# Kernel optimization log

Measured on AMD Instinct MI355X. Metric: run time of the kernel, lower is better.

The kernel has to match this reference:

```python
import jax, jax.numpy as jnp
import numpy as np

B, V, C, D = 32, 64, 32, 256
VOCAB = 20000
NUM_T = 1000


def _run_lstm(x, Wih, Whh, b):
    # x: [T, B, H_in]; torch-style single-layer LSTM with zero initial state
    T, Bb, _ = x.shape
    H = Whh.shape[1]
    def step(carry, xt):
        h, c = carry
        z = xt @ Wih.T + h @ Whh.T + b
        i, f, g, o = jnp.split(z, 4, axis=-1)
        c = jax.nn.sigmoid(f) * c + jax.nn.sigmoid(i) * jnp.tanh(g)
        h = jax.nn.sigmoid(o) * jnp.tanh(c)
        return (h, c), h
    h0 = jnp.zeros((Bb, H), x.dtype)
    _, ys = jax.lax.scan(step, (h0, h0), x)
    return ys


def _forward(input_seqs, masks, lengths, seq_time_step, code_masks, emb, WQ1, WK1,
             decay, initial, lstm_Wih, lstm_Whh, lstm_b, hs_Wih, hs_Whh, hs_b,
             whk_W, whk_b, w1_W, w1_b, w2_W, w2_b, fuse_W, fuse_b, lab_W, lab_b,
             betas, Wdiff, diffusion_time_t, normal_noise):
    Bb, Vv, Cc = input_seqs.shape
    tok = input_seqs.reshape(-1, Cc)                      # [B*V, C]
    x = emb[tok]                                          # [B*V, C, D]
    q = x @ WQ1.T
    k = x @ WK1.T
    dp = jnp.einsum('bcd,bed->bce', q, k)                 # [B*V, C, C]
    cm = code_masks.reshape(-1, Cc)
    dp = dp - cm[:, None, :] - cm[:, :, None]
    sp = jax.nn.softmax(dp / jnp.sqrt(jnp.float32(D)), axis=-1)
    femb = jnp.einsum('bce,bed->bcd', sp, x)              # attended code embeddings
    femb = ((cm - 1e20) / -1e20)[:, :, None] * femb       # zero out padded codes
    dec = decay[tok][..., None]                           # [B*V, C, 1]
    ini = initial[tok][..., None]
    t = seq_time_step.reshape(-1)[:, None, None]          # [B*V, 1, 1]
    gate = jax.nn.sigmoid(dec * t + ini)                  # time-decay gate
    vv = jnp.einsum('bcx,bcd->bd', gate, femb)            # [B*V, D] visit vector
    vv = vv.reshape(Bb, Vv, -1).transpose(1, 0, 2)        # [V, B, D]

    lstm_out = _run_lstm(vv, lstm_Wih, lstm_Whh, lstm_b)  # [V, B, D]
    t_lstm = lstm_out.transpose(1, 0, 2)                  # [B, V, D]
    hiddenstate = _run_lstm(lstm_out, hs_Wih, hs_Whh, hs_b).transpose(1, 0, 2)

    # Vectorized form of the original per-step python loop.
    # NOTE: the original always uses e_k = t_lstm_out[:, 0:1, :] (step 0) -- kept faithfully.
    e_k = t_lstm[:, 0:1, :]                               # [B, 1, D]
    whp = hiddenstate[:, :-1, :] @ whk_W.T + whk_b        # [B, V-1, D]
    cat = jnp.concatenate([jnp.broadcast_to(e_k, whp.shape), whp], axis=-1)
    attn = jax.nn.softmax(jnp.tanh(cat @ w1_W.T + w1_b) @ w2_W.T + w2_b, axis=-1)
    rest = e_k * attn[..., 0:1] + whp * attn[..., 1:2]
    aligned = jnp.concatenate([e_k, rest], axis=1)        # [B, V, D]

    alpha = jnp.cumprod(1.0 - betas)[diffusion_time_t][:, None, None]
    noisy = aligned * jnp.sqrt(alpha) + normal_noise * jnp.sqrt(1.0 - alpha)
    predicted_noise = noisy @ Wdiff                       # surrogate for UNetModel (source not provided)
    gen = aligned + (normal_noise - predicted_noise)

    fused = jnp.concatenate([t_lstm, gen], axis=-1) @ fuse_W.T + fuse_b   # [B, V, D]
    mask_final = (jnp.arange(Vv)[None, :] == (lengths - 1)[:, None]).astype(fused.dtype)
    final = (fused * mask_final[:, :, None]).sum(axis=1)  # select last valid visit
    return final @ lab_W.T + lab_b                        # [B, 2]


def setup_inputs() -> dict:
    key = jax.random.key(0)
    ks = jax.random.split(key, 20)
    s = 0.05
    n = lambda i, shp: jax.random.normal(ks[i], shp, jnp.float32) * s
    emb = jax.random.normal(ks[0], (VOCAB + 1, D), jnp.float32) * 0.02
    emb = emb.at[VOCAB].set(0.0)  # padding_idx row
    return {
        'input_seqs': jax.random.randint(ks[1], (B, V, C), 0, VOCAB),
        'masks': jnp.zeros((B, V), jnp.float32),
        'lengths': jax.random.randint(ks[2], (B,), 1, V + 1),
        'seq_time_step': jax.random.uniform(ks[3], (B, V), jnp.float32),
        'code_masks': jnp.zeros((B, V, C), jnp.float32),
        'emb': emb,
        'WQ1': n(4, (D, D)), 'WK1': n(5, (D, D)),
        'decay': jnp.full((VOCAB + 1,), -0.1, jnp.float32),
        'initial': jnp.full((VOCAB + 1,), 1.0, jnp.float32),
        'lstm_Wih': n(6, (4 * D, D)), 'lstm_Whh': n(7, (4 * D, D)),
        'lstm_b': jnp.zeros((4 * D,), jnp.float32),
        'hs_Wih': n(8, (4 * D, D)), 'hs_Whh': n(9, (4 * D, D)),
        'hs_b': jnp.zeros((4 * D,), jnp.float32),
        'whk_W': n(10, (D, D)), 'whk_b': jnp.zeros((D,), jnp.float32),
        'w1_W': n(11, (64, 2 * D)), 'w1_b': jnp.zeros((64,), jnp.float32),
        'w2_W': n(12, (2, 64)), 'w2_b': jnp.zeros((2,), jnp.float32),
        'fuse_W': n(13, (D, 2 * D)), 'fuse_b': jnp.zeros((D,), jnp.float32),
        'lab_W': n(14, (2, D)), 'lab_b': jnp.zeros((2,), jnp.float32),
        'betas': jnp.linspace(1e-4, 0.02, NUM_T, dtype=jnp.float32),
        'Wdiff': n(15, (D, D)),
        'diffusion_time_t': jax.random.randint(ks[16], (B,), 0, NUM_T),
        'normal_noise': jax.random.normal(ks[17], (B, V, D), jnp.float32),
    }


def reference(input_seqs, masks, lengths, seq_time_step, code_masks, emb, WQ1, WK1,
              decay, initial, lstm_Wih, lstm_Whh, lstm_b, hs_Wih, hs_Whh, hs_b,
              whk_W, whk_b, w1_W, w1_b, w2_W, w2_b, fuse_W, fuse_b, lab_W, lab_b,
              betas, Wdiff, diffusion_time_t, normal_noise):
    return _forward(input_seqs, masks, lengths, seq_time_step, code_masks, emb, WQ1, WK1,
                    decay, initial, lstm_Wih, lstm_Whh, lstm_b, hs_Wih, hs_Whh, hs_b,
                    whk_W, whk_b, w1_W, w1_b, w2_W, w2_b, fuse_W, fuse_b, lab_W, lab_b,
                    betas, Wdiff, diffusion_time_t, normal_noise)
```

## Files before the change

### kernel.cpp

```cpp
#include <hip/hip_runtime.h>
#include <hip/hip_bf16.h>
#include <cmath>

typedef __attribute__((ext_vector_type(8))) short bf16x8;
typedef __attribute__((ext_vector_type(4))) float f32x4;
typedef __attribute__((ext_vector_type(4))) int i32x4;
typedef __attribute__((ext_vector_type(2))) unsigned int u32x2;

__device__ __forceinline__ float bf2f(unsigned short u) {
    unsigned int x = ((unsigned int)u) << 16;
    return __builtin_bit_cast(float, x);
}
__device__ __forceinline__ unsigned short f2bf(float f) {
    unsigned int x = __builtin_bit_cast(unsigned int, f);
    unsigned int lsb = (x >> 16) & 1u;
    x += 0x7fffu + lsb;
    return (unsigned short)(x >> 16);
}
__device__ __forceinline__ float sigm(float z) {
    return 1.f / (1.f + __expf(-z));
}
__device__ __forceinline__ float rcpf(float x) { return __builtin_amdgcn_rcpf(x); }
__device__ __forceinline__ float sigm_f(float z) { return rcpf(1.f + __expf(-z)); }
__device__ __forceinline__ float tanh_f(float z) { return 1.f - 2.f * rcpf(1.f + __expf(2.f * z)); }

__device__ __forceinline__ long ldg_sc8l(const void* p) {
    long r;
    asm volatile("global_load_dwordx2 %0, %1, off sc1" : "=v"(r) : "v"(p) : "memory");
    return r;
}
__device__ __forceinline__ u32x2 ldg_sc_u2(const void* p) {
    u32x2 r;
    asm volatile("global_load_dwordx2 %0, %1, off sc1" : "=v"(r) : "v"(p) : "memory");
    return r;
}
__device__ __forceinline__ void stg_sc_u2(void* p, u32x2 v) {
    asm volatile("global_store_dwordx2 %0, %1, off sc1" :: "v"(p), "v"(v) : "memory");
}
__device__ __forceinline__ void stg_sc_b(void* p, int v) {
    asm volatile("global_store_byte %0, %1, off sc1" :: "v"(p), "v"(v) : "memory");
}

__global__ void __launch_bounds__(256) pack_all(
    const float* __restrict__ Whh1, const float* __restrict__ Wih2,
    const float* __restrict__ Whh2, const float* __restrict__ Wih1,
    const float* __restrict__ WQ1, const float* __restrict__ WK1,
    const float* __restrict__ betas, const int* __restrict__ dift,
    const float* __restrict__ whk_W, const float* __restrict__ fuse_W,
    const float* __restrict__ w1_W,
    long* __restrict__ Wq, float* __restrict__ cs,
    unsigned short* __restrict__ W1h, unsigned short* __restrict__ M_pk,
    float* __restrict__ alpha, int* __restrict__ flags,
    float* __restrict__ whkT, float* __restrict__ fuseT,
    float* __restrict__ w1T) {
    int blk = blockIdx.x, tid = threadIdx.x;
    if (blk < 384) {
        int R = blk * 8 + (tid >> 5);
        int mat = R >> 10;
        int n = R & 1023;
        int t32 = tid & 31;
        const float* src = (mat == 0) ? Whh1 : (mat == 1 ? Wih2 : Whh2);
        const float* rp = src + (size_t)n * 256 + t32 * 8;
        float v[8];
        float mx = 0.f;
        for (int j = 0; j < 8; ++j) { v[j] = rp[j]; mx = fmaxf(mx, fabsf(v[j])); }
        for (int m = 1; m <= 16; m <<= 1) mx = fmaxf(mx, __shfl_xor(mx, m));
        float inv = mx > 0.f ? 127.f / mx : 0.f;
        unsigned int lo = 0, hi = 0;
        for (int j = 0; j < 4; ++j) {
            int iv = __float2int_rn(v[j] * inv);
            lo |= ((unsigned int)(unsigned char)(signed char)iv) << (8 * j);
            int iv2 = __float2int_rn(v[4 + j] * inv);
            hi |= ((unsigned int)(unsigned char)(signed char)iv2) << (8 * j);
        }
        int g = n >> 8, rem = n & 255;
        int w8 = rem >> 5, dt = (rem >> 4) & 1, cc = rem & 15;
        int t8 = g * 2 + dt;
        int kb = t32 >> 2, q = t32 & 3;
        unsigned int* dst = (unsigned int*)Wq +
            ((size_t)((mat * 512 + w8 * 64 + t8 * 8 + kb) * 64) + q * 16 + cc) * 2;
        dst[0] = lo;
        dst[1] = hi;
        if (t32 == 0) cs[mat * 1024 + n] = mx / 16129.f;
    } else if (blk < 512) {
        int cch = (blk - 384) * 256 + tid;
        int nt = cch >> 9;
        int r = cch & 511;
        int kb = r >> 6;
        int lane = r & 63;
        int grow = nt * 16 + (lane & 15);
        int k0 = kb * 32 + (lane >> 4) * 8;
        const float* sp = Wih1 + (size_t)grow * 256 + k0;
        bf16x8 hi;
        for (int j = 0; j < 8; ++j) hi[j] = (short)f2bf(sp[j]);
        *reinterpret_cast<bf16x8*>(W1h + (size_t)cch * 8) = hi;
    } else if (blk == 512) {
        if (tid < 32) {
            int tb = dift[tid];
            float p = 1.f;
            for (int i = 0; i <= tb; ++i) p *= (1.f - betas[i]);
            alpha[tid] = p;
        }
    } else if (blk == 513) {
        for (int i = tid; i < 2048; i += 256) flags[i] = 0;
    } else if (blk < 578) {
        int gid = (blk - 514) * 256 + tid;
        for (int i = 0; i < 4; ++i) {
            int e = gid + i * 16384;
            int k = e >> 8, dd = e & 255;
            whkT[e] = whk_W[(size_t)dd * 256 + k];
        }
    } else if (blk < 706) {
        int gid = (blk - 578) * 256 + tid;
        for (int i = 0; i < 4; ++i) {
            int e = gid + i * 32768;
            int k = e >> 8, dd = e & 255;
            fuseT[e] = fuse_W[(size_t)dd * 512 + k];
        }
    } else if (blk < 738) {
        int gid = (blk - 706) * 256 + tid;
        for (int i = 0; i < 4; ++i) {
            int e = gid + i * 8192;
            int k = e >> 6, j = e & 63;
            w1T[e] = w1_W[(size_t)j * 512 + k];
        }
    } else {
        __shared__ unsigned short As[256][32];
        __shared__ unsigned short Bs[256][32];
        int bx = blk - 738;
        int e0 = (bx >> 3) << 5;
        int f0 = (bx & 7) << 5;
        int col = tid & 31, rr = tid >> 5;
        for (int rep = 0; rep < 32; ++rep) {
            int d = rep * 8 + rr;
            As[d][col] = f2bf(WQ1[d * 256 + e0 + col]);
            Bs[d][col] = f2bf(WK1[d * 256 + f0 + col]);
        }
        __syncthreads();
        int el = tid & 31;
        int fl0 = tid >> 5;
        for (int i = 0; i < 4; ++i) {
            int fl = fl0 + 8 * i;
            float acc = 0.f;
            for (int d = 0; d < 256; ++d)
                acc += bf2f(As[d][el]) * bf2f(Bs[d][fl]);
            int e = e0 + el, f = f0 + fl;
            int kb = e >> 5, r = (e >> 3) & 3, j = e & 7;
            int nb = f >> 4;
            int lane = (r << 4) | (f & 15);
            M_pk[(((nb * 8 + kb) * 64) + lane) * 8 + j] = f2bf(acc);
        }
    }
}

__global__ void __launch_bounds__(256) attn_bags(
    const int* __restrict__ seqs, const float* __restrict__ tstep,
    const float* __restrict__ cmask, const float* __restrict__ emb,
    const float* __restrict__ decay, const float* __restrict__ initial,
    const unsigned short* __restrict__ M_pk, float* __restrict__ vv) {
    __shared__ __align__(16) unsigned short x_bf[32 * 256];
    __shared__ __align__(16) unsigned short t1_bf[32 * 256];
    __shared__ float dp_f[32 * 33];
    __shared__ float gate_sh[32];
    __shared__ float cm_sh[32];
    __shared__ int tok_sh[32];
    __shared__ float w_sh[32];

    int bag = blockIdx.x;
    int tid = threadIdx.x;

    if (tid < 32) {
        int tok = seqs[bag * 32 + tid];
        tok_sh[tid] = tok;
        float cm = cmask[bag * 32 + tid];
        cm_sh[tid] = cm;
        float tt = tstep[bag];
        float g = sigm(decay[tok] * tt + initial[tok]);
        g *= (cm - 1e20f) / (-1e20f);
        gate_sh[tid] = g;
    }
    __syncthreads();

    for (int it = 0; it < 8; ++it) {
        int fidx = it * 256 + tid;
        int c = fidx >> 6;
        int f4 = fidx & 63;
        const float4* src = reinterpret_cast<const float4*>(emb + (size_t)tok_sh[c] * 256) + f4;
        float4 vx = *src;
        int colx = f4 * 4;
        int eidx = c * 256 + (colx ^ ((c & 7) << 3));
        ushort4 w;
        w.x = f2bf(vx.x); w.y = f2bf(vx.y); w.z = f2bf(vx.z); w.w = f2bf(vx.w);
        *reinterpret_cast<ushort4*>(&x_bf[eidx]) = w;
    }
    __syncthreads();

    int wv = tid >> 6;
    int lane = tid & 63;
    int lr = lane & 15;
    int lk = lane >> 4;

    f32x4 acc[2][4];
    for (int a = 0; a < 2; ++a)
        for (int n = 0; n < 4; ++n) acc[a][n] = (f32x4){0.f, 0.f, 0.f, 0.f};
    for (int kb = 0; kb < 8; ++kb) {
        bf16x8 afr[2];
        for (int mb = 0; mb < 2; ++mb) {
            int row = mb * 16 + lr;
            int colx = kb * 32 + lk * 8;
            afr[mb] = *reinterpret_cast<const bf16x8*>(&x_bf[row * 256 + (colx ^ ((row & 7) << 3))]);
        }
        for (int nbi = 0; nbi < 4; ++nbi) {
            int nb = wv * 4 + nbi;
            bf16x8 bfr = *reinterpret_cast<const bf16x8*>(M_pk + (((nb * 8 + kb) * 64) + lane) * 8);
            acc[0][nbi] = __builtin_amdgcn_mfma_f32_16x16x32_bf16(afr[0], bfr, acc[0][nbi], 0, 0, 0);
            acc[1][nbi] = __builtin_amdgcn_mfma_f32_16x16x32_bf16(afr[1], bfr, acc[1][nbi], 0, 0, 0);
        }
    }
    for (int mb = 0; mb < 2; ++mb)
        for (int nbi = 0; nbi < 4; ++nbi)
            for (int r = 0; r < 4; ++r) {
                int row = mb * 16 + lk * 4 + r;
                int colx = wv * 64 + nbi * 16 + lr;
                t1_bf[row * 256 + (colx ^ ((row & 7) << 3))] = f2bf(acc[mb][nbi][r]);
            }
    __syncthreads();

    {
        int mb = wv >> 1, nb2 = wv & 1;
        f32x4 dacc = (f32x4){0.f, 0.f, 0.f, 0.f};
        for (int kb = 0; kb < 8; ++kb) {
            int cola = kb * 32 + lk * 8;
            int rowa = mb * 16 + lr;
            bf16x8 afr = *reinterpret_cast<const bf16x8*>(&t1_bf[rowa * 256 + (cola ^ ((rowa & 7) << 3))]);
            int rowb = nb2 * 16 + lr;
            bf16x8 bfr = *reinterpret_cast<const bf16x8*>(&x_bf[rowb * 256 + (cola ^ ((rowb & 7) << 3))]);
            dacc = __builtin_amdgcn_mfma_f32_16x16x32_bf16(afr, bfr, dacc, 0, 0, 0);
        }
        for (int r = 0; r < 4; ++r) {
            int c = mb * 16 + lk * 4 + r;
            int e = nb2 * 16 + lr;
            dp_f[c * 33 + e] = dacc[r];
        }
    }
    __syncthreads();

    if (tid < 32) {
        int c = tid;
        float cmc = cm_sh[c];
        float lg[32];
        float mx = -1e30f;
        for (int e = 0; e < 32; ++e) {
            float l = (dp_f[c * 33 + e] - cmc - cm_sh[e]) * 0.0625f;
            lg[e] = l;
            mx = fmaxf(mx, l);
        }
        float s = 0.f;
        for (int e = 0; e < 32; ++e) { float ex = __expf(lg[e] - mx); lg[e] = ex; s += ex; }
        float inv = 1.f / s;
        for (int e = 0; e < 32; ++e) dp_f[c * 33 + e] = lg[e] * inv;
    }
    __syncthreads();
    if (tid < 32) {
        int e = tid;
        float a2 = 0.f;
        for (int c = 0; c < 32; ++c) a2 += gate_sh[c] * dp_f[c * 33 + e];
        w_sh[e] = a2;
    }
    __syncthreads();

    float accv = 0.f;
    int d = tid;
    for (int e = 0; e < 32; ++e)
        accv += w_sh[e] * bf2f(x_bf[e * 256 + (d ^ ((e & 7) << 3))]);
    vv[(size_t)bag * 256 + d] = accv;
}

__global__ void __launch_bounds__(256) x1_mfma(const float* __restrict__ vv,
                                               const unsigned short* __restrict__ W1h,
                                               const float* __restrict__ lstm_b,
                                               unsigned short* __restrict__ X1bf) {
    __shared__ __align__(16) unsigned short xs[32 * 256];
    int blk = blockIdx.x;
    int rb = blk >> 3, gb = blk & 7;
    int tid = threadIdx.x;
    for (int it = 0; it < 8; ++it) {
        int idx = it * 256 + tid;
        int row = idx >> 6, f4 = idx & 63;
        float4 v = *reinterpret_cast<const float4*>(vv + (size_t)(rb * 32 + row) * 256 + f4 * 4);
        ushort4 w;
        w.x = f2bf(v.x); w.y = f2bf(v.y); w.z = f2bf(v.z); w.w = f2bf(v.w);
        *reinterpret_cast<ushort4*>(&xs[row * 256 + ((f4 * 4) ^ ((row & 7) << 3))]) = w;
    }
    __syncthreads();
    int wv = tid >> 6, lane = tid & 63, cl = lane & 15, kh = lane >> 4;
    f32x4 acc[2][2];
    for (int n = 0; n < 2; ++n) {
        int nt = gb * 8 + wv * 2 + n;
        float bz = lstm_b[nt * 16 + cl];
        acc[n][0] = (f32x4){bz, bz, bz, bz};
        acc[n][1] = (f32x4){bz, bz, bz, bz};
    }
    #pragma unroll
    for (int kb = 0; kb < 8; ++kb) {
        int k = kb * 32 + kh * 8;
        bf16x8 a0 = *reinterpret_cast<const bf16x8*>(&xs[cl * 256 + (k ^ ((cl & 7) << 3))]);
        bf16x8 a1 = *reinterpret_cast<const bf16x8*>(&xs[(16 + cl) * 256 + (k ^ (((16 + cl) & 7) << 3))]);
        for (int n = 0; n < 2; ++n) {
            int nt = gb * 8 + wv * 2 + n;
            size_t o = ((size_t)(nt * 8 + kb) * 64 + lane) * 8;
            bf16x8 bh = *reinterpret_cast<const bf16x8*>(W1h + o);
            acc[n][0] = __builtin_amdgcn_mfma_f32_16x16x32_bf16(a0, bh, acc[n][0], 0, 0, 0);
            acc[n][1] = __builtin_amdgcn_mfma_f32_16x16x32_bf16(a1, bh, acc[n][1], 0, 0, 0);
        }
    }
    for (int n = 0; n < 2; ++n) {
        int nt = gb * 8 + wv * 2 + n;
        int g = nt * 16 + cl;
        int dX = g & 255, gt = g >> 8;
        for (int mt = 0; mt < 2; ++mt)
            for (int r = 0; r < 4; ++r) {
                int row = rb * 32 + mt * 16 + kh * 4 + r;
                int b = row >> 6, t = row & 63;
                X1bf[((size_t)t * 32 + b) * 1024 + dX * 4 + gt] = f2bf(acc[n][mt][r]);
            }
    }
}

__global__ void __launch_bounds__(512, 2) lstm_persist(
    const long* __restrict__ Wq, const float* __restrict__ cs,
    const unsigned short* __restrict__ X1bf, const float* __restrict__ hs_b,
    unsigned short* __restrict__ h1bf, unsigned short* __restrict__ h2bf,
    signed char* h1q, unsigned short* p1, int* flags) {
    int role = blockIdx.x;
    int half = role & 1;
    int kind = role >> 1;
    int tid = threadIdx.x;
    int w = tid >> 6, lane = tid & 63, c = lane & 15, q = lane >> 4;

    long wt[64];
    #pragma unroll
    for (int t8 = 0; t8 < 8; ++t8)
        #pragma unroll
        for (int kb = 0; kb < 8; ++kb)
            wt[t8 * 8 + kb] = Wq[(size_t)((kind * 512 + w * 64 + t8 * 8 + kb) * 64) + lane];
    float csv[8];
    #pragma unroll
    for (int t8 = 0; t8 < 8; ++t8) {
        int g = t8 >> 1, dt = t8 & 1;
        csv[t8] = cs[kind * 1024 + g * 256 + w * 32 + dt * 16 + c];
    }

    if (kind == 0) {
        __shared__ signed char hq[2][16][272];
        float cstate[8] = {0.f, 0.f, 0.f, 0.f, 0.f, 0.f, 0.f, 0.f};
        int B0 = half * 16 + q * 4;
        int dbase = w * 32;
        for (int t = 0; t < 64; ++t) {
            ushort4 xv[8];
            #pragma unroll
            for (int dt = 0; dt < 2; ++dt)
                #pragma unroll
                for (int r = 0; r < 4; ++r) {
                    int B = B0 + r, d = dbase + dt * 16 + c;
                    xv[dt * 4 + r] = *reinterpret_cast<const ushort4*>(
                        X1bf + ((size_t)(t * 32 + B) * 1024 + d * 4));
                }
            i32x4 acc[8];
            #pragma unroll
            for (int i = 0; i < 8; ++i) acc[i] = (i32x4){0, 0, 0, 0};
            if (t > 0) {
                int pb = (t - 1) & 1;
                long a[8];
                #pragma unroll
                for (int kb = 0; kb < 8; ++kb)
                    a[kb] = *reinterpret_cast<const long*>(&hq[pb][c][kb * 32 + q * 8]);
                #pragma unroll
                for (int t8 = 0; t8 < 8; ++t8)
                    #pragma unroll
                    for (int kb = 0; kb < 8; ++kb)
                        acc[t8] = __builtin_amdgcn_mfma_i32_16x16x32_i8(
                            a[kb], wt[t8 * 8 + kb], acc[t8], 0, 0, 0);
            }
            #pragma unroll
            for (int dt = 0; dt < 2; ++dt)
                #pragma unroll
                for (int r = 0; r < 4; ++r) {
                    int idx = dt * 4 + r;
                    ushort4 x = xv[idx];
                    float zi = (float)acc[0 + dt][r] * csv[0 + dt] + bf2f(x.x);
                    float zf = (float)acc[2 + dt][r] * csv[2 + dt] + bf2f(x.y);
                    float zg = (float)acc[4 + dt][r] * csv[4 + dt] + bf2f(x.z);
                    float zo = (float)acc[6 + dt][r] * csv[6 + dt] + bf2f(x.w);
                    float cn = sigm_f(zf) * cstate[idx] + sigm_f(zi) * tanh_f(zg);
                    float hn = sigm_f(zo) * tanh_f(cn);
                    cstate[idx] = cn;
                    int B = B0 + r, d = dbase + dt * 16 + c;
                    h1bf[(size_t)(t * 32 + B) * 256 + d] = f2bf(hn);
                    int hv = __float2int_rn(hn * 127.f);
                    hq[t & 1][q * 4 + r][d] = (signed char)hv;
                    stg_sc_b(h1q + (size_t)(t * 32 + B) * 256 + d, hv);
                }
            asm volatile("s_waitcnt vmcnt(0)" ::: "memory");
            if (lane == 0)
                __hip_atomic_store(flags + t * 16 + half * 8 + w, 1,
                                   __ATOMIC_RELAXED, __HIP_MEMORY_SCOPE_AGENT);
            __syncthreads();
        }
    } else if (kind == 1) {
        for (int s = 0; s < 64; ++s) {
            const int* f = flags + s * 16 + half * 8;
            while (1) {
                int v = 1;
                if (lane < 8)
                    v = __hip_atomic_load(f + lane, __ATOMIC_RELAXED, __HIP_MEMORY_SCOPE_AGENT);
                if (__all(v != 0)) break;
                __builtin_amdgcn_s_sleep(1);
            }
            __builtin_amdgcn_sched_barrier(0);
            const signed char* hb = h1q + (size_t)(s * 32 + half * 16) * 256;
            long a[8];
            #pragma unroll
            for (int kb = 0; kb < 8; ++kb)
                a[kb] = ldg_sc8l(hb + c * 256 + kb * 32 + q * 8);
            asm volatile("s_waitcnt vmcnt(0)" ::: "memory");
            __builtin_amdgcn_sched_barrier(0);
            i32x4 acc[8];
            #pragma unroll
            for (int i = 0; i < 8; ++i) acc[i] = (i32x4){0, 0, 0, 0};
            #pragma unroll
            for (int t8 = 0; t8 < 8; ++t8)
                #pragma unroll
                for (int kb = 0; kb < 8; ++kb)
                    acc[t8] = __builtin_amdgcn_mfma_i32_16x16x32_i8(
                        a[kb], wt[t8 * 8 + kb], acc[t8], 0, 0, 0);
            #pragma unroll
            for (int t8 = 0; t8 < 8; ++t8) {
                int g = t8 >> 1, dt = t8 & 1;
                int n = g * 256 + w * 32 + dt * 16 + c;
                u32x2 pv;
                pv.x = (unsigned int)f2bf((float)acc[t8][0] * csv[t8]) |
                       ((unsigned int)f2bf((float)acc[t8][1] * csv[t8]) << 16);
                pv.y = (unsigned int)f2bf((float)acc[t8][2] * csv[t8]) |
                       ((unsigned int)f2bf((float)acc[t8][3] * csv[t8]) << 16);
                stg_sc_u2(p1 + ((size_t)(s * 2 + half) * 1024 + n) * 16 + q * 4, pv);
            }
            asm volatile("s_waitcnt vmcnt(0)" ::: "memory");
            if (lane == 0)
                __hip_atomic_store(flags + 1024 + s * 16 + half * 8 + w, 1,
                                   __ATOMIC_RELAXED, __HIP_MEMORY_SCOPE_AGENT);
        }
    } else {
        __shared__ signed char hq2[2][16][272];
        float cstate[8] = {0.f, 0.f, 0.f, 0.f, 0.f, 0.f, 0.f, 0.f};
        float bias[8];
        #pragma unroll
        for (int t8 = 0; t8 < 8; ++t8) {
            int g = t8 >> 1, dt = t8 & 1;
            bias[t8] = hs_b[g * 256 + w * 32 + dt * 16 + c];
        }
        int B0 = half * 16 + q * 4;
        int dbase = w * 32;
        for (int s = 0; s < 64; ++s) {
            const int* fp = flags + 1024 + s * 16 + half * 8 + w;
            while (__hip_atomic_load(fp, __ATOMIC_RELAXED, __HIP_MEMORY_SCOPE_AGENT) == 0)
                __builtin_amdgcn_s_sleep(1);
            __builtin_amdgcn_sched_barrier(0);
            u32x2 pv[8];
            #pragma unroll
            for (int t8 = 0; t8 < 8; ++t8) {
                int g = t8 >> 1, dt = t8 & 1;
                int n = g * 256 + w * 32 + dt * 16 + c;
                pv[t8] = ldg_sc_u2(p1 + ((size_t)(s * 2 + half) * 1024 + n) * 16 + q * 4);
            }
            i32x4 acc[8];
            #pragma unroll
            for (int i = 0; i < 8; ++i) acc[i] = (i32x4){0, 0, 0, 0};
            if (s > 0) {
                int pb = (s - 1) & 1;
                long a[8];
                #pragma unroll
                for (int kb = 0; kb < 8; ++kb)
                    a[kb] = *reinterpret_cast<const long*>(&hq2[pb][c][kb * 32 + q * 8]);
                asm volatile("s_waitcnt vmcnt(0)" ::: "memory");
                __builtin_amdgcn_sched_barrier(0);
                #pragma unroll
                for (int t8 = 0; t8 < 8; ++t8)
                    #pragma unroll
                    for (int kb = 0; kb < 8; ++kb)
                        acc[t8] = __builtin_amdgcn_mfma_i32_16x16x32_i8(
                            a[kb], wt[t8 * 8 + kb], acc[t8], 0, 0, 0);
            } else {
                asm volatile("s_waitcnt vmcnt(0)" ::: "memory");
                __builtin_amdgcn_sched_barrier(0);
            }
            #pragma unroll
            for (int dt = 0; dt < 2; ++dt)
                #pragma unroll
                for (int r = 0; r < 4; ++r) {
                    int idx = dt * 4 + r;
                    float p_i = bf2f((unsigned short)((r < 2 ? pv[0 + dt].x : pv[0 + dt].y) >> ((r & 1) * 16)));
                    float p_f = bf2f((unsigned short)((r < 2 ? pv[2 + dt].x : pv[2 + dt].y) >> ((r & 1) * 16)));
                    float p_g = bf2f((unsigned short)((r < 2 ? pv[4 + dt].x : pv[4 + dt].y) >> ((r & 1) * 16)));
                    float p_o = bf2f((unsigned short)((r < 2 ? pv[6 + dt].x : pv[6 + dt].y) >> ((r & 1) * 16)));
                    float zi = (float)acc[0 + dt][r] * csv[0 + dt] + p_i + bias[0 + dt];
                    float zf = (float)acc[2 + dt][r] * csv[2 + dt] + p_f + bias[2 + dt];
                    float zg = (float)acc[4 + dt][r] * csv[4 + dt] + p_g + bias[4 + dt];
                    float zo = (float)acc[6 + dt][r] * csv[6 + dt] + p_o + bias[6 + dt];
                    float cn = sigm_f(zf) * cstate[idx] + sigm_f(zi) * tanh_f(zg);
                    float hn = sigm_f(zo) * tanh_f(cn);
                    cstate[idx] = cn;
                    int B = B0 + r, d = dbase + dt * 16 + c;
                    h2bf[(size_t)(s * 32 + B) * 256 + d] = f2bf(hn);
                    hq2[s & 1][q * 4 + r][d] = (signed char)__float2int_rn(hn * 127.f);
                }
            __syncthreads();
        }
    }
}

__global__ void __launch_bounds__(256) tail_k(
    const int* __restrict__ lengths,
    const unsigned short* __restrict__ h1, const unsigned short* __restrict__ h2,
    const float* __restrict__ whkT, const float* __restrict__ whk_b,
    const float* __restrict__ w1T, const float* __restrict__ w1_b,
    const float* __restrict__ w2_W, const float* __restrict__ w2_b,
    const float* __restrict__ fuseT, const float* __restrict__ fuse_b,
    const float* __restrict__ lab_W, const float* __restrict__ lab_b,
    const float* __restrict__ Wdiff, const float* __restrict__ alpha,
    const float* __restrict__ noise, float* __restrict__ out) {
    __shared__ float ek[256], tv[256], hs[256], whp[256], a1s[64];
    __shared__ float noisy_s[256], fin[512], fused_s[256], attn_s[2];
    int b = blockIdx.x, tid = threadIdx.x;
    int vstar = lengths[b] - 1;
    {
        ek[tid] = bf2f(h1[(size_t)b * 256 + tid]);
        tv[tid] = bf2f(h1[((size_t)vstar * 32 + b) * 256 + tid]);
        if (vstar > 0)
            hs[tid] = bf2f(h2[((size_t)(vstar - 1) * 32 + b) * 256 + tid]);
    }
    __syncthreads();

    float aligned;
    if (vstar > 0) {
        float s0 = 0.f, s1 = 0.f, s2 = 0.f, s3 = 0.f;
        for (int k = 0; k < 256; k += 4) {
            s0 += whkT[(k + 0) * 256 + tid] * hs[k + 0];
            s1 += whkT[(k + 1) * 256 + tid] * hs[k + 1];
            s2 += whkT[(k + 2) * 256 + tid] * hs[k + 2];
            s3 += whkT[(k + 3) * 256 + tid] * hs[k + 3];
        }
        whp[tid] = whk_b[tid] + s0 + s1 + s2 + s3;
        __syncthreads();
        if (tid < 64) {
            float a0 = 0.f, a1 = 0.f, a2 = 0.f, a3 = 0.f;
            for (int k = 0; k < 256; k += 4) {
                a0 += w1T[(k + 0) * 64 + tid] * ek[k + 0];
                a1 += w1T[(k + 1) * 64 + tid] * ek[k + 1];
                a2 += w1T[(k + 2) * 64 + tid] * ek[k + 2];
                a3 += w1T[(k + 3) * 64 + tid] * ek[k + 3];
            }
            for (int k = 0; k < 256; k += 4) {
                a0 += w1T[(256 + k + 0) * 64 + tid] * whp[k + 0];
                a1 += w1T[(256 + k + 1) * 64 + tid] * whp[k + 1];
                a2 += w1T[(256 + k + 2) * 64 + tid] * whp[k + 2];
                a3 += w1T[(256 + k + 3) * 64 + tid] * whp[k + 3];
            }
            a1s[tid] = tanhf(w1_b[tid] + a0 + a1 + a2 + a3);
        }
        __syncthreads();
        if (tid < 2) {
            float a3 = w2_b[tid];
            const float* wr2 = w2_W + tid * 64;
            for (int k = 0; k < 64; ++k) a3 += wr2[k] * a1s[k];
            attn_s[tid] = a3;
        }
        __syncthreads();
        float m = fmaxf(attn_s[0], attn_s[1]);
        float e0 = __expf(attn_s[0] - m), e1 = __expf(attn_s[1] - m);
        float inv = 1.f / (e0 + e1);
        aligned = ek[tid] * (e0 * inv) + whp[tid] * (e1 * inv);
    } else {
        aligned = ek[tid];
    }

    float al = alpha[b];
    float sa = sqrtf(al), sb = sqrtf(1.f - al);
    float nz = noise[((size_t)b * 64 + vstar) * 256 + tid];
    noisy_s[tid] = aligned * sa + nz * sb;
    __syncthreads();
    {
        float p0 = 0.f, p1v = 0.f, p2 = 0.f, p3 = 0.f;
        for (int k = 0; k < 256; k += 4) {
            p0 += noisy_s[k + 0] * Wdiff[(size_t)(k + 0) * 256 + tid];
            p1v += noisy_s[k + 1] * Wdiff[(size_t)(k + 1) * 256 + tid];
            p2 += noisy_s[k + 2] * Wdiff[(size_t)(k + 2) * 256 + tid];
            p3 += noisy_s[k + 3] * Wdiff[(size_t)(k + 3) * 256 + tid];
        }
        float gen = aligned + nz - (p0 + p1v + p2 + p3);
        fin[tid] = tv[tid];
        fin[256 + tid] = gen;
    }
    __syncthreads();
    {
        float f0 = 0.f, f1 = 0.f, f2 = 0.f, f3 = 0.f;
        for (int k = 0; k < 512; k += 4) {
            f0 += fuseT[(k + 0) * 256 + tid] * fin[k + 0];
            f1 += fuseT[(k + 1) * 256 + tid] * fin[k + 1];
            f2 += fuseT[(k + 2) * 256 + tid] * fin[k + 2];
            f3 += fuseT[(k + 3) * 256 + tid] * fin[k + 3];
        }
        fused_s[tid] = fuse_b[tid] + f0 + f1 + f2 + f3;
    }
    __syncthreads();
    if (tid < 2) {
        float o = lab_b[tid];
        const float* lw = lab_W + tid * 256;
        for (int k = 0; k < 256; ++k) o += lw[k] * fused_s[k];
        out[b * 2 + tid] = o;
    }
}

extern "C" void kernel_launch(void* const* d_in, const int* in_sizes, int n_in,
                              void* d_out, int out_size, void* d_ws, size_t ws_size,
                              hipStream_t stream) {
    const int*   seqs    = (const int*)  d_in[0];
    const int*   lengths = (const int*)  d_in[2];
    const float* tstep   = (const float*)d_in[3];
    const float* cmask   = (const float*)d_in[4];
    const float* emb     = (const float*)d_in[5];
    const float* WQ1     = (const float*)d_in[6];
    const float* WK1     = (const float*)d_in[7];
    const float* decay   = (const float*)d_in[8];
    const float* initial = (const float*)d_in[9];
    const float* Wih1    = (const float*)d_in[10];
    const float* Whh1    = (const float*)d_in[11];
    const float* lstm_b  = (const float*)d_in[12];
    const float* Wih2    = (const float*)d_in[13];
    const float* Whh2    = (const float*)d_in[14];
    const float* hs_b    = (const float*)d_in[15];
    const float* whk_W   = (const float*)d_in[16];
    const float* whk_b   = (const float*)d_in[17];
    const float* w1_W    = (const float*)d_in[18];
    const float* w1_b    = (const float*)d_in[19];
    const float* w2_W    = (const float*)d_in[20];
    const float* w2_b    = (const float*)d_in[21];
    const float* fuse_W  = (const float*)d_in[22];
    const float* fuse_b  = (const float*)d_in[23];
    const float* lab_W   = (const float*)d_in[24];
    const float* lab_b   = (const float*)d_in[25];
    const float* betas   = (const float*)d_in[26];
    const float* Wdiff   = (const float*)d_in[27];
    const int*   dift    = (const int*)  d_in[28];
    const float* noise   = (const float*)d_in[29];
    float* out = (float*)d_out;

    float* ws = (float*)d_ws;
    size_t off = 0;
    auto alloc = [&](size_t nfloats) { size_t r = off; off += (nfloats + 63) & ~(size_t)63; return r; };
    unsigned short* M_pk  = (unsigned short*)(ws + alloc(32768));
    float*          alpha = ws + alloc(64);
    float*          cs    = ws + alloc(3072);
    int*            flags = (int*)(ws + alloc(2048));
    float*          vv    = ws + alloc(524288);
    unsigned short* X1bf  = (unsigned short*)(ws + alloc(1048576));
    unsigned short* h1bf  = (unsigned short*)(ws + alloc(262144));
    unsigned short* h2bf  = (unsigned short*)(ws + alloc(262144));
    unsigned short* p1    = (unsigned short*)(ws + alloc(1048576));
    long*           Wq    = (long*)(ws + alloc(196608));
    unsigned short* W1h   = (unsigned short*)(ws + alloc(131072));
    float*          whkT  = ws + alloc(65536);
    float*          fuseT = ws + alloc(131072);
    float*          w1T   = ws + alloc(32768);
    signed char*    h1q   = (signed char*)vv;

    pack_all<<<802, 256, 0, stream>>>(Whh1, Wih2, Whh2, Wih1, WQ1, WK1, betas, dift,
                                      whk_W, fuse_W, w1_W,
                                      Wq, cs, W1h, M_pk, alpha, flags,
                                      whkT, fuseT, w1T);
    attn_bags<<<2048, 256, 0, stream>>>(seqs, tstep, cmask, emb, decay, initial, M_pk, vv);
    x1_mfma<<<512, 256, 0, stream>>>(vv, W1h, lstm_b, X1bf);
    lstm_persist<<<6, 512, 0, stream>>>(Wq, cs, X1bf, hs_b, h1bf, h2bf, h1q, p1, flags);
    tail_k<<<32, 256, 0, stream>>>(lengths, h1bf, h2bf, whkT, whk_b,
                                   w1T, w1_b, w2_W, w2_b, fuseT, fuse_b,
                                   lab_W, lab_b, Wdiff, alpha, noise, out);
}
```

Before: 340.9 us.

## Precompute projected embedding table once instead of per-bag token projections

```diff
diff --git a/kernel.cpp b/kernel.cpp
--- a/kernel.cpp
+++ b/kernel.cpp
@@ -102,7 +102,7 @@
             alpha[tid] = p;
         }
     } else if (blk == 513) {
-        for (int i = tid; i < 2048; i += 256) flags[i] = 0;
+        for (int i = tid; i < 4096; i += 256) flags[i] = 0;
     } else if (blk < 578) {
         int gid = (blk - 514) * 256 + tid;
         for (int i = 0; i < 4; ++i) {
@@ -153,11 +153,59 @@
     }
 }
 
+__global__ void __launch_bounds__(256) eprep(const float* __restrict__ emb,
+                                             const unsigned short* __restrict__ M_pk,
+                                             unsigned short* __restrict__ Ep) {
+    __shared__ __align__(16) unsigned short x_bf[32 * 256];
+    int v0 = blockIdx.x * 32;
+    int tid = threadIdx.x;
+    for (int it = 0; it < 8; ++it) {
+        int fidx = it * 256 + tid;
+        int cc = fidx >> 6;
+        int f4 = fidx & 63;
+        int row = v0 + cc;
+        float4 vx = make_float4(0.f, 0.f, 0.f, 0.f);
+        if (row < 20001)
+            vx = *(reinterpret_cast<const float4*>(emb + (size_t)row * 256) + f4);
+        int colx = f4 * 4;
+        ushort4 w;
+        w.x = f2bf(vx.x); w.y = f2bf(vx.y); w.z = f2bf(vx.z); w.w = f2bf(vx.w);
+        *reinterpret_cast<ushort4*>(&x_bf[cc * 256 + (colx ^ ((cc & 7) << 3))]) = w;
+    }
+    __syncthreads();
+    int wv = tid >> 6, lane = tid & 63, lr = lane & 15, lk = lane >> 4;
+    f32x4 acc[2][4];
+    for (int a = 0; a < 2; ++a)
+        for (int n = 0; n < 4; ++n) acc[a][n] = (f32x4){0.f, 0.f, 0.f, 0.f};
+    for (int kb = 0; kb < 8; ++kb) {
+        bf16x8 afr[2];
+        for (int mb = 0; mb < 2; ++mb) {
+            int row = mb * 16 + lr;
+            int colx = kb * 32 + lk * 8;
+            afr[mb] = *reinterpret_cast<const bf16x8*>(&x_bf[row * 256 + (colx ^ ((row & 7) << 3))]);
+        }
+        for (int nbi = 0; nbi < 4; ++nbi) {
+            int nb = wv * 4 + nbi;
+            bf16x8 bfr = *reinterpret_cast<const bf16x8*>(M_pk + (((nb * 8 + kb) * 64) + lane) * 8);
+            acc[0][nbi] = __builtin_amdgcn_mfma_f32_16x16x32_bf16(afr[0], bfr, acc[0][nbi], 0, 0, 0);
+            acc[1][nbi] = __builtin_amdgcn_mfma_f32_16x16x32_bf16(afr[1], bfr, acc[1][nbi], 0, 0, 0);
+        }
+    }
+    for (int mb = 0; mb < 2; ++mb)
+        for (int nbi = 0; nbi < 4; ++nbi)
+            for (int r = 0; r < 4; ++r) {
+                int row = mb * 16 + lk * 4 + r;
+                int col = wv * 64 + nbi * 16 + lr;
+                if (v0 + row < 20001)
+                    Ep[(size_t)(v0 + row) * 256 + col] = f2bf(acc[mb][nbi][r]);
+            }
+}
+
 __global__ void __launch_bounds__(256) attn_bags(
     const int* __restrict__ seqs, const float* __restrict__ tstep,
     const float* __restrict__ cmask, const float* __restrict__ emb,
     const float* __restrict__ decay, const float* __restrict__ initial,
-    const unsigned short* __restrict__ M_pk, float* __restrict__ vv) {
+    const unsigned short* __restrict__ Ep, float* __restrict__ vv) {
     __shared__ __align__(16) unsigned short x_bf[32 * 256];
     __shared__ __align__(16) unsigned short t1_bf[32 * 256];
     __shared__ float dp_f[32 * 33];
@@ -193,38 +241,19 @@
         w.x = f2bf(vx.x); w.y = f2bf(vx.y); w.z = f2bf(vx.z); w.w = f2bf(vx.w);
         *reinterpret_cast<ushort4*>(&x_bf[eidx]) = w;
     }
+    for (int it = 0; it < 4; ++it) {
+        int idx = it * 256 + tid;
+        int cc = idx >> 5;
+        int colx = (idx & 31) * 8;
+        bf16x8 e = *reinterpret_cast<const bf16x8*>(Ep + (size_t)tok_sh[cc] * 256 + colx);
+        *reinterpret_cast<bf16x8*>(&t1_bf[cc * 256 + (colx ^ ((cc & 7) << 3))]) = e;
+    }
     __syncthreads();
 
     int wv = tid >> 6;
     int lane = tid & 63;
     int lr = lane & 15;
     int lk = lane >> 4;
-
-    f32x4 acc[2][4];
-    for (int a = 0; a < 2; ++a)
-        for (int n = 0; n < 4; ++n) acc[a][n] = (f32x4){0.f, 0.f, 0.f, 0.f};
-    for (int kb = 0; kb < 8; ++kb) {
-        bf16x8 afr[2];
-        for (int mb = 0; mb < 2; ++mb) {
-            int row = mb * 16 + lr;
-            int colx = kb * 32 + lk * 8;
-            afr[mb] = *reinterpret_cast<const bf16x8*>(&x_bf[row * 256 + (colx ^ ((row & 7) << 3))]);
-        }
-        for (int nbi = 0; nbi < 4; ++nbi) {
-            int nb = wv * 4 + nbi;
-            bf16x8 bfr = *reinterpret_cast<const bf16x8*>(M_pk + (((nb * 8 + kb) * 64) + lane) * 8);
-            acc[0][nbi] = __builtin_amdgcn_mfma_f32_16x16x32_bf16(afr[0], bfr, acc[0][nbi], 0, 0, 0);
-            acc[1][nbi] = __builtin_amdgcn_mfma_f32_16x16x32_bf16(afr[1], bfr, acc[1][nbi], 0, 0, 0);
-        }
-    }
-    for (int mb = 0; mb < 2; ++mb)
-        for (int nbi = 0; nbi < 4; ++nbi)
-            for (int r = 0; r < 4; ++r) {
-                int row = mb * 16 + lk * 4 + r;
-                int colx = wv * 64 + nbi * 16 + lr;
-                t1_bf[row * 256 + (colx ^ ((row & 7) << 3))] = f2bf(acc[mb][nbi][r]);
-            }
-    __syncthreads();
 
     {
         int mb = wv >> 1, nb2 = wv & 1;
@@ -661,7 +690,7 @@
     unsigned short* M_pk  = (unsigned short*)(ws + alloc(32768));
     float*          alpha = ws + alloc(64);
     float*          cs    = ws + alloc(3072);
-    int*            flags = (int*)(ws + alloc(2048));
+    int*            flags = (int*)(ws + alloc(4096));
     float*          vv    = ws + alloc(524288);
     unsigned short* X1bf  = (unsigned short*)(ws + alloc(1048576));
     unsigned short* h1bf  = (unsigned short*)(ws + alloc(262144));
@@ -672,13 +701,15 @@
     float*          whkT  = ws + alloc(65536);
     float*          fuseT = ws + alloc(131072);
     float*          w1T   = ws + alloc(32768);
-    signed char*    h1q   = (signed char*)vv;
+    signed char*    h1q   = (signed char*)(ws + alloc(131072));
+    unsigned short* Ep    = (unsigned short*)(ws + alloc(2560128));
 
     pack_all<<<802, 256, 0, stream>>>(Whh1, Wih2, Whh2, Wih1, WQ1, WK1, betas, dift,
                                       whk_W, fuse_W, w1_W,
                                       Wq, cs, W1h, M_pk, alpha, flags,
                                       whkT, fuseT, w1T);
-    attn_bags<<<2048, 256, 0, stream>>>(seqs, tstep, cmask, emb, decay, initial, M_pk, vv);
+    eprep<<<626, 256, 0, stream>>>(emb, M_pk, Ep);
+    attn_bags<<<2048, 256, 0, stream>>>(seqs, tstep, cmask, emb, decay, initial, Ep, vv);
     x1_mfma<<<512, 256, 0, stream>>>(vv, W1h, lstm_b, X1bf);
     lstm_persist<<<6, 512, 0, stream>>>(Wq, cs, X1bf, hs_b, h1bf, h2bf, h1q, p1, flags);
     tail_k<<<32, 256, 0, stream>>>(lengths, h1bf, h2bf, whkT, whk_b,
```

Measured after the change: 350.4 us (median of 2 runs). +2.8%, slower.
